# Performance work log

Measured on AMD Instinct MI355X. Metric: run time of the kernel, lower is better.

## Reference

```python
import jax, jax.numpy as jnp
import numpy as np

S, E, K, D = 50000, 20000, 128, 64
NUM_LAYER = 3
E1, E0 = 1000000, 1000000  # nnz of pos / neg adjacency
B = 4096


def _edges(key, n_rows, n_cols, n_edges):
    k1, k2, k3 = jax.random.split(key, 3)
    rows = jax.random.randint(k1, (n_edges,), 0, n_rows)
    cols = jax.random.randint(k2, (n_edges,), 0, n_cols)
    vals = jax.random.uniform(k3, (n_edges,), jnp.float32, 0.0, 0.1)
    return rows, cols, vals


def setup_inputs() -> dict:
    key = jax.random.key(0)
    ks = jax.random.split(key, 32)
    inp = {}
    inp['stu_id'] = jax.random.randint(ks[0], (B,), 0, S)
    inp['exer_id'] = jax.random.randint(ks[1], (B,), 0, E)
    inp['kn_emb'] = (jax.random.uniform(ks[2], (B, K)) < 0.1).astype(jnp.float32)
    # embeddings
    inp['stu_emb'] = jax.random.normal(ks[3], (S, D), jnp.float32) * 0.1
    inp['exer_emb'] = jax.random.normal(ks[4], (E, D), jnp.float32) * 0.1
    inp['kn_base'] = jax.random.normal(ks[5], (K, D), jnp.float32) * 0.1
    inp['stu_bias'] = jax.random.normal(ks[6], (S, 1), jnp.float32) * 0.1
    inp['e_disc'] = jax.random.normal(ks[7], (E, 1), jnp.float32) * 0.1
    # GCN linear layers
    inp['W1_w'] = jax.random.normal(ks[8], (K, K), jnp.float32) * (1.0 / np.sqrt(K))
    inp['W1_b'] = jnp.zeros((K,), jnp.float32)
    inp['W0_w'] = jax.random.normal(ks[9], (K, K), jnp.float32) * (1.0 / np.sqrt(K))
    inp['W0_b'] = jnp.zeros((K,), jnp.float32)
    # PosLinear prednet
    inp['pn1_w'] = jax.random.normal(ks[10], (256, K), jnp.float32) * 0.05
    inp['pn1_b'] = jnp.zeros((256,), jnp.float32)
    inp['pn2_w'] = jax.random.normal(ks[11], (128, 256), jnp.float32) * 0.05
    inp['pn2_b'] = jnp.zeros((128,), jnp.float32)
    inp['pn3_w'] = jax.random.normal(ks[12], (1, 128), jnp.float32) * 0.05
    inp['pn3_b'] = jnp.zeros((1,), jnp.float32)
    # sparse adjacencies (COO) pos(1) / neg(0), user->item and item->user
    r, c, v = _edges(ks[13], S, E, E1)
    inp['ui1_r'], inp['ui1_c'], inp['ui1_v'] = r, c, v
    r, c, v = _edges(ks[14], E, S, E1)
    inp['iu1_r'], inp['iu1_c'], inp['iu1_v'] = r, c, v
    r, c, v = _edges(ks[15], S, E, E0)
    inp['ui0_r'], inp['ui0_c'], inp['ui0_v'] = r, c, v
    r, c, v = _edges(ks[16], E, S, E0)
    inp['iu0_r'], inp['iu0_c'], inp['iu0_v'] = r, c, v
    # self-loop degree normalizers (1/(deg+1)-style positive scalars)
    inp['d_i_1'] = jax.random.uniform(ks[17], (S,), jnp.float32, 0.01, 1.0)
    inp['d_j_1'] = jax.random.uniform(ks[18], (E,), jnp.float32, 0.01, 1.0)
    inp['d_i_0'] = jax.random.uniform(ks[19], (S,), jnp.float32, 0.01, 1.0)
    inp['d_j_0'] = jax.random.uniform(ks[20], (E,), jnp.float32, 0.01, 1.0)
    return inp


def _spmm(rows, cols, vals, x, n_rows):
    # sparse [n_rows, n_cols] @ dense [n_cols, K]
    return jax.ops.segment_sum(vals[:, None] * x[cols], rows, num_segments=n_rows)


def _poslinear(x, w, b):
    wp = 2.0 * jax.nn.relu(-w) + w  # == |w|, as in PosLinear
    return x @ wp.T + b


def reference(stu_id, exer_id, kn_emb, stu_emb, exer_emb, kn_base, stu_bias, e_disc,
              W1_w, W1_b, W0_w, W0_b, pn1_w, pn1_b, pn2_w, pn2_b, pn3_w, pn3_b,
              ui1_r, ui1_c, ui1_v, iu1_r, iu1_c, iu1_v,
              ui0_r, ui0_c, ui0_v, iu0_r, iu0_c, iu0_v,
              d_i_1, d_j_1, d_i_0, d_j_0):
    # project embeddings onto knowledge space: [S,K], [E,K]
    stat = stu_emb @ kn_base.T
    kdiff = exer_emb @ kn_base.T
    for _ in range(NUM_LAYER):
        u1 = _spmm(ui1_r, ui1_c, ui1_v, kdiff, S) + stat * d_i_1[:, None]
        u1 = u1 @ W1_w.T + W1_b
        i1 = _spmm(iu1_r, iu1_c, iu1_v, stat, E) + kdiff * d_j_1[:, None]
        i1 = i1 @ W1_w.T + W1_b
        u0 = _spmm(ui0_r, ui0_c, ui0_v, kdiff, S) + stat * d_i_0[:, None]
        u0 = u0 @ W0_w.T + W0_b
        i0 = _spmm(iu0_r, iu0_c, iu0_v, stat, E) + kdiff * d_j_0[:, None]
        i0 = i0 @ W0_w.T + W0_b
        stat = u1 + u0
        kdiff = i1 + i0
    # diagnosis head (NCD-style), dropout in eval mode -> identity
    stat_b = jax.nn.sigmoid(stat[stu_id] + stu_bias[stu_id])      # [B,K]
    k_d = jax.nn.sigmoid(kdiff[exer_id])                           # [B,K]
    disc = jax.nn.sigmoid(e_disc[exer_id])                         # [B,1]
    x = disc * (stat_b - k_d) * kn_emb
    x = jax.nn.sigmoid(_poslinear(x, pn1_w, pn1_b))
    x = jax.nn.sigmoid(_poslinear(x, pn2_w, pn2_b))
    out = jax.nn.sigmoid(_poslinear(x, pn3_w, pn3_b)).reshape(-1)
    return out
```

## Files before the change

kernel.cpp:

```cpp
#include <hip/hip_runtime.h>
#include <hip/hip_bf16.h>

#define SN 50000
#define EN 20000
#define KN 128
#define DN 64
#define BN 4096
#define NE 1000000
#define NLAYER 3

#define CH_SHIFT 12
#define NCH0 5
#define NCH1 13
#define SIDE1_BASE2 (2 * SN * NCH0)
#define NTOT2 (2 * (SN * NCH0 + EN * NCH1))

#define BIN_SHIFT 11
#define NBIN2 ((NTOT2 + 2047) >> 11)
#define T1 4096
#define PG1 ((NE + T1 - 1) / T1)
#define HB 256

typedef float f32x4 __attribute__((ext_vector_type(4)));
typedef float f32x2 __attribute__((ext_vector_type(2)));
typedef short bf16x8 __attribute__((ext_vector_type(8)));

__device__ __forceinline__ float sigmoidf_(float v) { return 1.f / (1.f + __expf(-v)); }
__device__ __forceinline__ float bf_lo(unsigned u) { return __uint_as_float(u << 16); }
__device__ __forceinline__ float bf_hi(unsigned u) { return __uint_as_float(u & 0xffff0000u); }
__device__ __forceinline__ float bf_one(unsigned short s) { return __uint_as_float((unsigned)s << 16); }
__device__ __forceinline__ unsigned packbf2(float a, float b) {
    __hip_bfloat16 ha = __float2bfloat16(a), hb = __float2bfloat16(b);
    unsigned short ua = *(unsigned short*)&ha, ub = *(unsigned short*)&hb;
    return (unsigned)ua | ((unsigned)ub << 16);
}
__device__ __forceinline__ unsigned short packbf1(float a) {
    __hip_bfloat16 ha = __float2bfloat16(a);
    return *(unsigned short*)&ha;
}
__device__ __forceinline__ unsigned char fp8_of_bf16(unsigned short h) {
    float f = bf_one(h);
    int pk = __builtin_amdgcn_cvt_pk_fp8_f32(f, f, 0, false);
    return (unsigned char)(pk & 0xff);
}

struct CsrB {
    const int* rows[4]; const int* cols[4]; const float* vals[4];
};

__device__ __forceinline__ int bucket_idx(int a, int r, int cc) {
    int side = a >> 1;
    int nch = side ? NCH1 : NCH0;
    int base = side ? SIDE1_BASE2 : 0;
    int tb = a & 1;
    return base + (2 * r + tb) * nch + (cc >> CH_SHIFT);
}

__global__ __launch_bounds__(256) void hist_coarse(CsrB c, int* __restrict__ cnt) {
    __shared__ int h[512];
    const int t = threadIdx.x;
    h[t] = 0; h[t + 256] = 0;
    __syncthreads();
    const int a = blockIdx.x >> 8;
    const int tile = blockIdx.x & 255;
    const int per = (NE + HB - 1) / HB;
    const int beg = tile * per, end = min(beg + per, NE);
    for (int i = beg + t; i < end; i += 256)
        atomicAdd(&h[bucket_idx(a, c.rows[a][i], c.cols[a][i]) >> BIN_SHIFT], 1);
    __syncthreads();
    if (h[t]) atomicAdd(&cnt[t], h[t]);
    if (h[t + 256]) atomicAdd(&cnt[t + 256], h[t + 256]);
}

__global__ __launch_bounds__(512) void scan_coarse(const int* __restrict__ cnt,
                                                   int* __restrict__ base,
                                                   int* __restrict__ tails) {
    __shared__ int sh[512];
    const int t = threadIdx.x;
    const int v = (t < NBIN2) ? cnt[t] : 0;
    sh[t] = v;
    __syncthreads();
    for (int o = 1; o < 512; o <<= 1) {
        int x = sh[t]; int u = (t >= o) ? sh[t - o] : 0;
        __syncthreads(); sh[t] = x + u; __syncthreads();
    }
    if (t < NBIN2) {
        const int ex = sh[t] - v;
        base[t] = ex;
        tails[t] = ex;
    }
    if (t == 511) base[NBIN2] = sh[511];
}

__global__ __launch_bounds__(512) void part1(CsrB c, int* __restrict__ tails,
                                             int2* __restrict__ stg) {
    __shared__ int2 srec[T1];
    __shared__ unsigned short sbin[T1];
    __shared__ int h[512], offs[512], gbase[512], sc[512];
    const int t = threadIdx.x;
    const int a = blockIdx.x / PG1;
    const int tile = blockIdx.x - a * PG1;
    const int beg = tile * T1;
    const int cnt = min(T1, NE - beg);
    h[t] = 0;
    __syncthreads();

    int2 rec[8]; int rbin[8]; int rrank[8];
#pragma unroll
    for (int k = 0; k < 8; ++k) {
        int o = t + k * 512;
        if (o < cnt) {
            int i = beg + o;
            int cc = c.cols[a][i];
            int B = bucket_idx(a, c.rows[a][i], cc);
            int bin = B >> BIN_SHIFT;
            rec[k] = make_int2(cc | ((B & 2047) << 17), __float_as_int(c.vals[a][i]));
            rbin[k] = bin;
            rrank[k] = atomicAdd(&h[bin], 1);
        } else {
            rbin[k] = -1;
        }
    }
    __syncthreads();
    sc[t] = h[t];
    __syncthreads();
    for (int o = 1; o < 512; o <<= 1) {
        int x = sc[t]; int u = (t >= o) ? sc[t - o] : 0;
        __syncthreads(); sc[t] = x + u; __syncthreads();
    }
    offs[t] = sc[t] - h[t];
    if (h[t] > 0) gbase[t] = atomicAdd(&tails[t], h[t]);
    __syncthreads();
#pragma unroll
    for (int k = 0; k < 8; ++k) {
        if (rbin[k] >= 0) {
            int pos = offs[rbin[k]] + rrank[k];
            srec[pos] = rec[k];
            sbin[pos] = (unsigned short)rbin[k];
        }
    }
    __syncthreads();
    for (int idx = t; idx < cnt; idx += 512) {
        int b = sbin[idx];
        stg[gbase[b] + (idx - offs[b])] = srec[idx];
    }
}

__global__ __launch_bounds__(512) void part2(const int* __restrict__ coarseBase,
                                             const int2* __restrict__ stg,
                                             int* __restrict__ rp,
                                             int2* __restrict__ cv) {
    __shared__ int cnt2[2048];
    __shared__ int tsum[512];
    const int b = blockIdx.x;
    const int t = threadIdx.x;
    const int fineBase = b << BIN_SHIFT;
    const int nf = min(2048, NTOT2 - fineBase);
    const int segBeg = coarseBase[b];
    const int segEnd = coarseBase[b + 1];
    for (int i = t; i < 2048; i += 512) cnt2[i] = 0;
    __syncthreads();
    for (int e = segBeg + t; e < segEnd; e += 512)
        atomicAdd(&cnt2[((unsigned)stg[e].x) >> 17], 1);
    __syncthreads();
    const int i4 = t * 4;
    int v0 = cnt2[i4], v1 = cnt2[i4 + 1], v2 = cnt2[i4 + 2], v3 = cnt2[i4 + 3];
    tsum[t] = v0 + v1 + v2 + v3;
    __syncthreads();
    for (int o = 1; o < 512; o <<= 1) {
        int x = tsum[t]; int u = (t >= o) ? tsum[t - o] : 0;
        __syncthreads(); tsum[t] = x + u; __syncthreads();
    }
    const int pre = (t == 0) ? 0 : tsum[t - 1];
    const int p0 = pre, p1 = pre + v0, p2 = p1 + v1, p3 = p2 + v2;
    cnt2[i4] = p0; cnt2[i4 + 1] = p1; cnt2[i4 + 2] = p2; cnt2[i4 + 3] = p3;
    if (i4 + 0 < nf) rp[fineBase + i4 + 0] = segBeg + p0;
    if (i4 + 1 < nf) rp[fineBase + i4 + 1] = segBeg + p1;
    if (i4 + 2 < nf) rp[fineBase + i4 + 2] = segBeg + p2;
    if (i4 + 3 < nf) rp[fineBase + i4 + 3] = segBeg + p3;
    if (b == NBIN2 - 1 && t == 511) rp[NTOT2] = segEnd;
    __syncthreads();
    for (int e = segBeg + t; e < segEnd; e += 512) {
        int2 r = stg[e];
        int pos = segBeg + atomicAdd(&cnt2[((unsigned)r.x) >> 17], 1);
        cv[pos] = make_int2(r.x & 0xFFFF, r.y);
    }
}

__global__ __launch_bounds__(256) void f2bf3(
    const float* __restrict__ s0, unsigned short* __restrict__ d0, int n0,
    const float* __restrict__ s1, unsigned short* __restrict__ d1, int n1,
    const float* __restrict__ s2, unsigned short* __restrict__ d2, int n2) {
    int j = blockIdx.x * 256 + threadIdx.x;
    const float* s; unsigned short* d;
    if (j < n0) { s = s0; d = d0; }
    else {
        j -= n0;
        if (j < n1) { s = s1; d = d1; }
        else {
            j -= n1;
            if (j >= n2) return;
            s = s2; d = d2;
        }
    }
    float2 f = ((const float2*)s)[j];
    ((unsigned*)d)[j] = packbf2(f.x, f.y);
}

template <int KK>
__global__ __launch_bounds__(256) void gemm_proj(const float* __restrict__ X,
                                                 const unsigned short* __restrict__ W,
                                                 unsigned short* __restrict__ out,
                                                 unsigned char* __restrict__ f8,
                                                 int M) {
    constexpr int PITCH = KK + 8;
    __shared__ unsigned short Wl[128 * PITCH];
    const int t = threadIdx.x;
    for (int idx = t * 8; idx < 128 * KK; idx += 2048) {
        int r = idx / KK, k = idx - r * KK;
        *(uint4*)(&Wl[r * PITCH + k]) = *(const uint4*)(&W[idx]);
    }
    __syncthreads();
    const int lane = t & 63;
    const int nm = lane & 15;
    const int quad = lane >> 4;
    const int row0 = blockIdx.x * 64 + (t >> 6) * 16;
    if (row0 >= M) return;

    f32x4 acc[8];
#pragma unroll
    for (int nt = 0; nt < 8; ++nt) acc[nt] = (f32x4){0.f, 0.f, 0.f, 0.f};

    const float* xrow = X + (size_t)(row0 + nm) * KK + quad * 8;
#pragma unroll
    for (int ks = 0; ks < KK / 32; ++ks) {
        float4 f0 = *(const float4*)(xrow + ks * 32);
        float4 f1 = *(const float4*)(xrow + ks * 32 + 4);
        unsigned q[4] = {packbf2(f0.x, f0.y), packbf2(f0.z, f0.w),
                         packbf2(f1.x, f1.y), packbf2(f1.z, f1.w)};
        bf16x8 a = *(bf16x8*)q;
#pragma unroll
        for (int nt = 0; nt < 8; ++nt) {
            bf16x8 b = *(const bf16x8*)(&Wl[(nt * 16 + nm) * PITCH + ks * 32 + quad * 8]);
            acc[nt] = __builtin_amdgcn_mfma_f32_16x16x32_bf16(a, b, acc[nt], 0, 0, 0);
        }
    }
    const size_t obase = (size_t)(row0 + quad * 4) * 128 + nm;
    unsigned short* orow = out + obase;
    unsigned char* frow = f8 + obase;
#pragma unroll
    for (int r = 0; r < 4; ++r)
#pragma unroll
        for (int nt = 0; nt < 8; ++nt) {
            unsigned short h = packbf1(acc[nt][r]);
            orow[(size_t)r * 128 + nt * 16] = h;
            frow[(size_t)r * 128 + nt * 16] = fp8_of_bf16(h);
        }
}

template <bool LIST>
__global__ __launch_bounds__(512) void gemm2_mfma(
    const unsigned short* __restrict__ agg1S, const unsigned short* __restrict__ agg0S,
    const unsigned short* __restrict__ yS,
    const float* __restrict__ d1S, const float* __restrict__ d0S,
    unsigned short* __restrict__ outS, unsigned char* __restrict__ f8S,
    const unsigned short* __restrict__ agg1E, const unsigned short* __restrict__ agg0E,
    const unsigned short* __restrict__ yE,
    const float* __restrict__ d1E, const float* __restrict__ d0E,
    unsigned short* __restrict__ outE, unsigned char* __restrict__ f8E,
    const unsigned short* __restrict__ W1, const unsigned short* __restrict__ W0,
    const float* __restrict__ b1, const float* __restrict__ b0,
    const int* __restrict__ idsS, const int* __restrict__ idsE, int nblkS) {
    constexpr int PITCH = 136;
    __shared__ unsigned short Wl[2 * 128 * PITCH];
    const int t = threadIdx.x;
    for (int idx = t * 8; idx < 128 * 128; idx += 4096) {
        int r = idx >> 7, k = idx & 127;
        *(uint4*)(&Wl[r * PITCH + k]) = *(const uint4*)(&W1[idx]);
        *(uint4*)(&Wl[128 * PITCH + r * PITCH + k]) = *(const uint4*)(&W0[idx]);
    }
    __syncthreads();
    const bool sideE = (int)blockIdx.x >= nblkS;
    const unsigned short* agg1 = sideE ? agg1E : agg1S;
    const unsigned short* agg0 = sideE ? agg0E : agg0S;
    const unsigned short* y    = sideE ? yE : yS;
    const float* d1 = sideE ? d1E : d1S;
    const float* d0 = sideE ? d0E : d0S;
    unsigned short* out = sideE ? outE : outS;
    unsigned char* f8 = sideE ? f8E : f8S;
    const int M = LIST ? BN : (sideE ? EN : SN);
    const int lane = t & 63;
    const int nm = lane & 15;
    const int quad = lane >> 4;
    const int row0 = ((int)blockIdx.x - (sideE ? nblkS : 0)) * 128 + (t >> 6) * 16;
    if (row0 >= M) return;

    const int lrow = row0 + nm;
    int grow = lrow;
    if (LIST) grow = (sideE ? idsE : idsS)[lrow];

    const float d1v = d1[grow];
    const float d0v = d0[grow];

    f32x4 acc[8];
#pragma unroll
    for (int nt = 0; nt < 8; ++nt) acc[nt] = (f32x4){0.f, 0.f, 0.f, 0.f};

    const size_t rbA = (size_t)lrow * 128 + quad * 8;
    const size_t rbY = (size_t)grow * 128 + quad * 8;
#pragma unroll
    for (int ks = 0; ks < 4; ++ks) {
        uint4 ua1 = *(const uint4*)(agg1 + rbA + ks * 32);
        uint4 ua0 = *(const uint4*)(agg0 + rbA + ks * 32);
        uint4 uy  = *(const uint4*)(y    + rbY + ks * 32);
        uint4 p1, p0;
        {
            unsigned* a1 = (unsigned*)&ua1; unsigned* a0 = (unsigned*)&ua0;
            unsigned* yy = (unsigned*)&uy;
            unsigned* q1 = (unsigned*)&p1; unsigned* q0 = (unsigned*)&p0;
#pragma unroll
            for (int w = 0; w < 4; ++w) {
                float ylo = bf_lo(yy[w]), yhi = bf_hi(yy[w]);
                q1[w] = packbf2(bf_lo(a1[w]) + d1v * ylo, bf_hi(a1[w]) + d1v * yhi);
                q0[w] = packbf2(bf_lo(a0[w]) + d0v * ylo, bf_hi(a0[w]) + d0v * yhi);
            }
        }
        bf16x8 af1 = *(bf16x8*)&p1;
        bf16x8 af0 = *(bf16x8*)&p0;
#pragma unroll
        for (int nt = 0; nt < 8; ++nt) {
            bf16x8 bw1 = *(const bf16x8*)(&Wl[(nt * 16 + nm) * PITCH + ks * 32 + quad * 8]);
            acc[nt] = __builtin_amdgcn_mfma_f32_16x16x32_bf16(af1, bw1, acc[nt], 0, 0, 0);
            bf16x8 bw0 = *(const bf16x8*)(&Wl[128 * PITCH + (nt * 16 + nm) * PITCH + ks * 32 + quad * 8]);
            acc[nt] = __builtin_amdgcn_mfma_f32_16x16x32_bf16(af0, bw0, acc[nt], 0, 0, 0);
        }
    }
    const size_t obase = (size_t)(row0 + quad * 4) * 128 + nm;
    unsigned short* orow = out + obase;
    unsigned char* frow = f8 + obase;
#pragma unroll
    for (int nt = 0; nt < 8; ++nt) {
        float bb = b1[nt * 16 + nm] + b0[nt * 16 + nm];
#pragma unroll
        for (int r = 0; r < 4; ++r) {
            unsigned short h = packbf1(acc[nt][r] + bb);
            orow[(size_t)r * 128 + nt * 16] = h;
            if (!LIST) frow[(size_t)r * 128 + nt * 16] = fp8_of_bf16(h);
        }
    }
}

template <bool LIST>
__global__ __launch_bounds__(256) void spmm_all(
    const int* __restrict__ rp, const long long* __restrict__ cv,
    const unsigned char* __restrict__ kd8, const unsigned char* __restrict__ st8,
    unsigned short* __restrict__ as1, unsigned short* __restrict__ as0,
    unsigned short* __restrict__ ae1, unsigned short* __restrict__ ae0,
    const int* __restrict__ idsS, const int* __restrict__ idsE) {
    const int wave = (blockIdx.x * 256 + threadIdx.x) >> 6;
    const int lane = threadIdx.x & 63;
    const int NW = LIST ? 2 * BN : SN + EN;
    if (wave >= NW) return;
    const bool sideE = LIST ? (wave >= BN) : (wave >= SN);
    const int li = sideE ? (wave - (LIST ? BN : SN)) : wave;
    const int r = LIST ? (sideE ? idsE[li] : idsS[li]) : li;
    const int nch = sideE ? NCH1 : NCH0;
    const int* rpb = rp + (sideE ? SIDE1_BASE2 : 0);
    const int q = lane >> 4;
    const int c = lane & 15;
    const unsigned char* g8 = (sideE ? st8 : kd8) + c * 8;

    const int rbase = 2 * r * nch;
    const int e0 = rpb[rbase];
    const int em = rpb[rbase + nch];
    const int ee = rpb[rbase + 2 * nch];

    f32x2 accP[4], accN[4];
#pragma unroll
    for (int j = 0; j < 4; ++j) { accP[j] = (f32x2){0.f, 0.f}; accN[j] = (f32x2){0.f, 0.f}; }

#define QUAD(E, ACC)                                                        \
    {                                                                       \
        int col = (int)((E) & 0xFFFF);                                      \
        float v = __int_as_float((int)((E) >> 32));                         \
        f32x2 vv = {v, v};                                                  \
        uint2 u = *(const uint2*)(g8 + (col << 7));                         \
        ACC[0] += vv * __builtin_amdgcn_cvt_pk_f32_fp8((int)u.x, false);    \
        ACC[1] += vv * __builtin_amdgcn_cvt_pk_f32_fp8((int)u.x, true);     \
        ACC[2] += vv * __builtin_amdgcn_cvt_pk_f32_fp8((int)u.y, false);    \
        ACC[3] += vv * __builtin_amdgcn_cvt_pk_f32_fp8((int)u.y, true);     \
    }

    {
        int e = e0;
        for (; e + 16 <= em; e += 16) {
            long long E0 = cv[e + q];
            long long E1 = cv[e + 4 + q];
            long long E2 = cv[e + 8 + q];
            long long E3 = cv[e + 12 + q];
            QUAD(E0, accP) QUAD(E1, accP) QUAD(E2, accP) QUAD(E3, accP)
        }
        for (; e + 4 <= em; e += 4) {
            long long E0 = cv[e + q];
            QUAD(E0, accP)
        }
        if (e < em) {
            int idx = min(e + q, em - 1);
            long long E0 = cv[idx];
            if (e + q >= em) E0 &= 0xFFFFLL;
            QUAD(E0, accP)
        }
    }
    {
        int e = em;
        for (; e + 16 <= ee; e += 16) {
            long long E0 = cv[e + q];
            long long E1 = cv[e + 4 + q];
            long long E2 = cv[e + 8 + q];
            long long E3 = cv[e + 12 + q];
            QUAD(E0, accN) QUAD(E1, accN) QUAD(E2, accN) QUAD(E3, accN)
        }
        for (; e + 4 <= ee; e += 4) {
            long long E0 = cv[e + q];
            QUAD(E0, accN)
        }
        if (e < ee) {
            int idx = min(e + q, ee - 1);
            long long E0 = cv[idx];
            if (e + q >= ee) E0 &= 0xFFFFLL;
            QUAD(E0, accN)
        }
    }
#undef QUAD

#pragma unroll
    for (int j = 0; j < 4; ++j) {
        accP[j].x += __shfl_xor(accP[j].x, 16);
        accP[j].y += __shfl_xor(accP[j].y, 16);
        accN[j].x += __shfl_xor(accN[j].x, 16);
        accN[j].y += __shfl_xor(accN[j].y, 16);
        accP[j].x += __shfl_xor(accP[j].x, 32);
        accP[j].y += __shfl_xor(accP[j].y, 32);
        accN[j].x += __shfl_xor(accN[j].x, 32);
        accN[j].y += __shfl_xor(accN[j].y, 32);
    }
    unsigned short* o1 = sideE ? ae1 : as1;
    unsigned short* o0 = sideE ? ae0 : as0;
    const int oi = LIST ? li : r;
    const int base = (oi << 7) + c * 8;
    if (q == 0) {
        uint4 w;
        w.x = packbf2(accP[0].x, accP[0].y);
        w.y = packbf2(accP[1].x, accP[1].y);
        w.z = packbf2(accP[2].x, accP[2].y);
        w.w = packbf2(accP[3].x, accP[3].y);
        *(uint4*)&o1[base] = w;
    } else if (q == 1) {
        uint4 w;
        w.x = packbf2(accN[0].x, accN[0].y);
        w.y = packbf2(accN[1].x, accN[1].y);
        w.z = packbf2(accN[2].x, accN[2].y);
        w.w = packbf2(accN[3].x, accN[3].y);
        *(uint4*)&o0[base] = w;
    }
}

template <int KK, int NCOLS, int ROWS, bool ABSW, bool SIG>
__global__ __launch_bounds__(256) void gemm_xwT(const float* __restrict__ X,
                                                const float* __restrict__ W,
                                                const float* __restrict__ bias,
                                                float* __restrict__ out, int M) {
    constexpr int KP = 32;
    constexpr int NG = 256 / NCOLS;
    constexpr int RT = ROWS / NG;
    __shared__ float BT[KP * (NCOLS + 1)];
    __shared__ float Xl[ROWS * (KK + 1)];
    const int t = threadIdx.x;
    const int j = t % NCOLS;
    const int rg = t / NCOLS;
    const int row0 = blockIdx.x * ROWS;

    for (int idx = t; idx < ROWS * KK; idx += 256) {
        int r = idx / KK, k = idx % KK;
        int gr = row0 + r;
        Xl[r * (KK + 1) + k] = (gr < M) ? X[gr * KK + k] : 0.f;
    }
    float acc[RT];
#pragma unroll
    for (int i = 0; i < RT; ++i) acc[i] = 0.f;

    for (int k0 = 0; k0 < KK; k0 += KP) {
        __syncthreads();
        for (int idx = t; idx < NCOLS * KP; idx += 256) {
            int jj = idx / KP, kp = idx % KP;
            float w = W[jj * KK + k0 + kp];
            BT[kp * (NCOLS + 1) + jj] = ABSW ? fabsf(w) : w;
        }
        __syncthreads();
#pragma unroll
        for (int kp = 0; kp < KP; ++kp) {
            float b = BT[kp * (NCOLS + 1) + j];
#pragma unroll
            for (int rr = 0; rr < RT; ++rr)
                acc[rr] += Xl[(rg * RT + rr) * (KK + 1) + k0 + kp] * b;
        }
    }
    float bj = bias ? bias[j] : 0.f;
#pragma unroll
    for (int rr = 0; rr < RT; ++rr) {
        int gr = row0 + rg * RT + rr;
        if (gr < M) {
            float v = acc[rr] + bj;
            out[gr * NCOLS + j] = SIG ? sigmoidf_(v) : v;
        }
    }
}

__global__ __launch_bounds__(128) void head1_kernel(
    const int* __restrict__ stu_id, const int* __restrict__ exer_id,
    const float* __restrict__ kn_emb, const unsigned short* __restrict__ statB,
    const unsigned short* __restrict__ kdB, const float* __restrict__ stu_bias,
    const float* __restrict__ e_disc, float* __restrict__ x) {
    const int b = blockIdx.x;
    const int k = threadIdx.x;
    const int sid = stu_id[b], eid = exer_id[b];
    float disc = sigmoidf_(e_disc[eid]);
    float sb = sigmoidf_(bf_one(statB[(b << 7) + k]) + stu_bias[sid]);
    float kd = sigmoidf_(bf_one(kdB[(b << 7) + k]));
    x[(b << 7) + k] = disc * (sb - kd) * kn_emb[(b << 7) + k];
}

__global__ __launch_bounds__(256) void pn3_kernel(const float* __restrict__ h2,
                                                  const float* __restrict__ w3,
                                                  const float* __restrict__ b3,
                                                  float* __restrict__ out) {
    __shared__ float wl[128];
    const int t = threadIdx.x;
    if (t < 128) wl[t] = fabsf(w3[t]);
    __syncthreads();
    const int b = blockIdx.x * 256 + t;
    float acc = 0.f;
#pragma unroll 4
    for (int k = 0; k < 128; ++k) acc += h2[(b << 7) + k] * wl[k];
    out[b] = sigmoidf_(acc + b3[0]);
}

static inline size_t align256(size_t x) { return (x + 255) & ~size_t(255); }

extern "C" void kernel_launch(void* const* d_in, const int* in_sizes, int n_in,
                              void* d_out, int out_size, void* d_ws, size_t ws_size,
                              hipStream_t stream) {
    const int*   stu_id   = (const int*)d_in[0];
    const int*   exer_id  = (const int*)d_in[1];
    const float* kn_emb   = (const float*)d_in[2];
    const float* stu_emb  = (const float*)d_in[3];
    const float* exer_emb = (const float*)d_in[4];
    const float* kn_base  = (const float*)d_in[5];
    const float* stu_bias = (const float*)d_in[6];
    const float* e_disc   = (const float*)d_in[7];
    const float* W1_w     = (const float*)d_in[8];
    const float* W1_b     = (const float*)d_in[9];
    const float* W0_w     = (const float*)d_in[10];
    const float* W0_b     = (const float*)d_in[11];
    const float* pn1_w    = (const float*)d_in[12];
    const float* pn1_b    = (const float*)d_in[13];
    const float* pn2_w    = (const float*)d_in[14];
    const float* pn2_b    = (const float*)d_in[15];
    const float* pn3_w    = (const float*)d_in[16];
    const float* pn3_b    = (const float*)d_in[17];
    const int*   ui1_r = (const int*)d_in[18]; const int* ui1_c = (const int*)d_in[19];
    const float* ui1_v = (const float*)d_in[20];
    const int*   iu1_r = (const int*)d_in[21]; const int* iu1_c = (const int*)d_in[22];
    const float* iu1_v = (const float*)d_in[23];
    const int*   ui0_r = (const int*)d_in[24]; const int* ui0_c = (const int*)d_in[25];
    const float* ui0_v = (const float*)d_in[26];
    const int*   iu0_r = (const int*)d_in[27]; const int* iu0_c = (const int*)d_in[28];
    const float* iu0_v = (const float*)d_in[29];
    const float* d_i_1 = (const float*)d_in[30];
    const float* d_j_1 = (const float*)d_in[31];
    const float* d_i_0 = (const float*)d_in[32];
    const float* d_j_0 = (const float*)d_in[33];
    float* out = (float*)d_out;

    typedef unsigned short u16;
    typedef unsigned char u8;
    char* p = (char*)d_ws;
    size_t off = 0;
    auto alloc = [&](size_t bytes) { char* q = p + off; off += align256(bytes); return q; };
    u16* stat  = (u16*)alloc(size_t(SN) * KN * 2);
    u16* kdiff = (u16*)alloc(size_t(EN) * KN * 2);
    u8* st8 = (u8*)alloc(size_t(SN) * KN);
    u8* kd8 = (u8*)alloc(size_t(EN) * KN);
    u16* as1 = (u16*)alloc(size_t(SN) * KN * 2);
    u16* as0 = (u16*)alloc(size_t(SN) * KN * 2);
    u16* ae1 = (u16*)alloc(size_t(EN) * KN * 2);
    u16* ae0 = (u16*)alloc(size_t(EN) * KN * 2);
    u16* statB = (u16*)alloc(size_t(BN) * KN * 2);
    u16* kdB   = (u16*)alloc(size_t(BN) * KN * 2);
    u16* Kb  = (u16*)alloc(size_t(KN) * DN * 2);
    u16* Wb1 = (u16*)alloc(size_t(KN) * KN * 2);
    u16* Wb0 = (u16*)alloc(size_t(KN) * KN * 2);
    int*  coarseCnt  = (int*)alloc(512 * 4);
    int*  coarseBase = (int*)alloc((NBIN2 + 1) * 4);
    int*  tails      = (int*)alloc(512 * 4);
    int*  rp_all     = (int*)alloc(size_t(NTOT2 + 1) * 4);
    int2* stg        = (int2*)alloc(size_t(4) * NE * 8);
    int2* cv_all     = (int2*)alloc(size_t(4) * NE * 8);
    float* xh = (float*)alloc(size_t(BN) * KN * 4);
    float* h1 = (float*)alloc(size_t(BN) * 256 * 4);
    float* h2 = (float*)alloc(size_t(BN) * 128 * 4);
    if (off > ws_size) return;

    CsrB c;
    c.rows[0] = ui1_r; c.cols[0] = ui1_c; c.vals[0] = ui1_v;
    c.rows[1] = ui0_r; c.cols[1] = ui0_c; c.vals[1] = ui0_v;
    c.rows[2] = iu1_r; c.cols[2] = iu1_c; c.vals[2] = iu1_v;
    c.rows[3] = iu0_r; c.cols[3] = iu0_c; c.vals[3] = iu0_v;

    hipMemsetAsync(coarseCnt, 0, 512 * 4, stream);
    hist_coarse<<<4 * HB, 256, 0, stream>>>(c, coarseCnt);
    scan_coarse<<<1, 512, 0, stream>>>(coarseCnt, coarseBase, tails);
    part1<<<4 * PG1, 512, 0, stream>>>(c, tails, stg);
    part2<<<NBIN2, 512, 0, stream>>>(coarseBase, stg, rp_all, cv_all);

    {
        const int n0 = KN * DN / 2, n1 = KN * KN / 2, n2 = KN * KN / 2;
        f2bf3<<<(n0 + n1 + n2 + 255) / 256, 256, 0, stream>>>(
            kn_base, Kb, n0, W1_w, Wb1, n1, W0_w, Wb0, n2);
    }

    gemm_proj<DN><<<(SN + 63) / 64, 256, 0, stream>>>(stu_emb, Kb, stat, st8, SN);
    gemm_proj<DN><<<(EN + 63) / 64, 256, 0, stream>>>(exer_emb, Kb, kdiff, kd8, EN);

    const int nblkS = (SN + 127) / 128, nblkE = (EN + 127) / 128;

    for (int l = 0; l < NLAYER; ++l) {
        if (l < NLAYER - 1) {
            spmm_all<false><<<(SN + EN + 3) / 4, 256, 0, stream>>>(
                rp_all, (const long long*)cv_all, kd8, st8, as1, as0, ae1, ae0,
                nullptr, nullptr);
            gemm2_mfma<false><<<nblkS + nblkE, 512, 0, stream>>>(
                as1, as0, stat, d_i_1, d_i_0, stat, st8,
                ae1, ae0, kdiff, d_j_1, d_j_0, kdiff, kd8,
                Wb1, Wb0, W1_b, W0_b, nullptr, nullptr, nblkS);
        } else {
            spmm_all<true><<<(2 * BN) / 4, 256, 0, stream>>>(
                rp_all, (const long long*)cv_all, kd8, st8, as1, as0, ae1, ae0,
                stu_id, exer_id);
            gemm2_mfma<true><<<2 * (BN / 128), 512, 0, stream>>>(
                as1, as0, stat, d_i_1, d_i_0, statB, nullptr,
                ae1, ae0, kdiff, d_j_1, d_j_0, kdB, nullptr,
                Wb1, Wb0, W1_b, W0_b, stu_id, exer_id, BN / 128);
        }
    }

    head1_kernel<<<BN, 128, 0, stream>>>(stu_id, exer_id, kn_emb, statB, kdB,
                                         stu_bias, e_disc, xh);
    gemm_xwT<128, 256, 16, true, true><<<BN / 16, 256, 0, stream>>>(xh, pn1_w, pn1_b, h1, BN);
    gemm_xwT<256, 128, 32, true, true><<<BN / 32, 256, 0, stream>>>(h1, pn2_w, pn2_b, h2, BN);
    pn3_kernel<<<BN / 256, 256, 0, stream>>>(h2, pn3_w, pn3_b, out);
    (void)out_size; (void)n_in; (void)in_sizes;
}
```

Measured before the change: 607.1 us.

## Fuse head kernels, merge projection GEMMs, fold memset into weight conversion

Folds the coarse-count memset into the weight-to-bf16 conversion kernel and merges the two projection GEMM launches into one grid covering both the student and exercise sides. Fuses the head elementwise step into the first prednet GEMM and the third linear layer into the second GEMM, which drops the xh and h2 intermediate buffers. The aim is fewer kernel launches and less global traffic in the small tail stages, at the cost of some extra shared memory and per-block work in the fused kernels.

```diff
diff --git a/kernel.cpp b/kernel.cpp
--- a/kernel.cpp
+++ b/kernel.cpp
@@ -187,11 +187,13 @@
     }
 }
 
-__global__ __launch_bounds__(256) void f2bf3(
+__global__ __launch_bounds__(256) void f2bf3z(
     const float* __restrict__ s0, unsigned short* __restrict__ d0, int n0,
     const float* __restrict__ s1, unsigned short* __restrict__ d1, int n1,
-    const float* __restrict__ s2, unsigned short* __restrict__ d2, int n2) {
+    const float* __restrict__ s2, unsigned short* __restrict__ d2, int n2,
+    int* __restrict__ coarseCnt) {
     int j = blockIdx.x * 256 + threadIdx.x;
+    if (j < 512) coarseCnt[j] = 0;
     const float* s; unsigned short* d;
     if (j < n0) { s = s0; d = d0; }
     else {
@@ -208,11 +210,12 @@
 }
 
 template <int KK>
-__global__ __launch_bounds__(256) void gemm_proj(const float* __restrict__ X,
-                                                 const unsigned short* __restrict__ W,
-                                                 unsigned short* __restrict__ out,
-                                                 unsigned char* __restrict__ f8,
-                                                 int M) {
+__global__ __launch_bounds__(256) void gemm_proj2(
+    const float* __restrict__ XS, const float* __restrict__ XE,
+    const unsigned short* __restrict__ W,
+    unsigned short* __restrict__ outS, unsigned char* __restrict__ f8S,
+    unsigned short* __restrict__ outE, unsigned char* __restrict__ f8E,
+    int nbS) {
     constexpr int PITCH = KK + 8;
     __shared__ unsigned short Wl[128 * PITCH];
     const int t = threadIdx.x;
@@ -221,10 +224,15 @@
         *(uint4*)(&Wl[r * PITCH + k]) = *(const uint4*)(&W[idx]);
     }
     __syncthreads();
+    const bool sideE = (int)blockIdx.x >= nbS;
+    const float* X = sideE ? XE : XS;
+    unsigned short* out = sideE ? outE : outS;
+    unsigned char* f8 = sideE ? f8E : f8S;
+    const int M = sideE ? EN : SN;
     const int lane = t & 63;
     const int nm = lane & 15;
     const int quad = lane >> 4;
-    const int row0 = blockIdx.x * 64 + (t >> 6) * 16;
+    const int row0 = ((int)blockIdx.x - (sideE ? nbS : 0)) * 64 + (t >> 6) * 16;
     if (row0 >= M) return;
 
     f32x4 acc[8];
@@ -465,26 +473,34 @@
     }
 }
 
-template <int KK, int NCOLS, int ROWS, bool ABSW, bool SIG>
-__global__ __launch_bounds__(256) void gemm_xwT(const float* __restrict__ X,
-                                                const float* __restrict__ W,
-                                                const float* __restrict__ bias,
-                                                float* __restrict__ out, int M) {
-    constexpr int KP = 32;
-    constexpr int NG = 256 / NCOLS;
-    constexpr int RT = ROWS / NG;
+__global__ __launch_bounds__(256) void pn1_fused(
+    const int* __restrict__ stu_id, const int* __restrict__ exer_id,
+    const float* __restrict__ kn_emb, const unsigned short* __restrict__ statB,
+    const unsigned short* __restrict__ kdB, const float* __restrict__ stu_bias,
+    const float* __restrict__ e_disc,
+    const float* __restrict__ W, const float* __restrict__ bias,
+    float* __restrict__ out) {
+    constexpr int KK = 128, NCOLS = 256, ROWS = 16, KP = 32;
+    constexpr int RT = 16;
     __shared__ float BT[KP * (NCOLS + 1)];
     __shared__ float Xl[ROWS * (KK + 1)];
-    const int t = threadIdx.x;
-    const int j = t % NCOLS;
-    const int rg = t / NCOLS;
+    __shared__ float sdisc[16], sbias[16];
+    const int t = threadIdx.x;
     const int row0 = blockIdx.x * ROWS;
-
+    if (t < 16) {
+        const int gr = row0 + t;
+        sdisc[t] = sigmoidf_(e_disc[exer_id[gr]]);
+        sbias[t] = stu_bias[stu_id[gr]];
+    }
+    __syncthreads();
     for (int idx = t; idx < ROWS * KK; idx += 256) {
-        int r = idx / KK, k = idx % KK;
-        int gr = row0 + r;
-        Xl[r * (KK + 1) + k] = (gr < M) ? X[gr * KK + k] : 0.f;
-    }
+        const int r = idx >> 7, k = idx & 127;
+        const int gr = row0 + r;
+        const float sb = sigmoidf_(bf_one(statB[(gr << 7) + k]) + sbias[r]);
+        const float kd = sigmoidf_(bf_one(kdB[(gr << 7) + k]));
+        Xl[r * (KK + 1) + k] = sdisc[r] * (sb - kd) * kn_emb[(gr << 7) + k];
+    }
+    const int j = t;
     float acc[RT];
 #pragma unroll
     for (int i = 0; i < RT; ++i) acc[i] = 0.f;
@@ -493,8 +509,7 @@
         __syncthreads();
         for (int idx = t; idx < NCOLS * KP; idx += 256) {
             int jj = idx / KP, kp = idx % KP;
-            float w = W[jj * KK + k0 + kp];
-            BT[kp * (NCOLS + 1) + jj] = ABSW ? fabsf(w) : w;
+            BT[kp * (NCOLS + 1) + jj] = fabsf(W[jj * KK + k0 + kp]);
         }
         __syncthreads();
 #pragma unroll
@@ -502,47 +517,65 @@
             float b = BT[kp * (NCOLS + 1) + j];
 #pragma unroll
             for (int rr = 0; rr < RT; ++rr)
+                acc[rr] += Xl[rr * (KK + 1) + k0 + kp] * b;
+        }
+    }
+    const float bj = bias[j];
+#pragma unroll
+    for (int rr = 0; rr < RT; ++rr)
+        out[(row0 + rr) * NCOLS + j] = sigmoidf_(acc[rr] + bj);
+}
+
+__global__ __launch_bounds__(256) void pn23_fused(
+    const float* __restrict__ X, const float* __restrict__ W,
+    const float* __restrict__ bias, const float* __restrict__ w3,
+    const float* __restrict__ b3, float* __restrict__ out) {
+    constexpr int KK = 256, NCOLS = 128, ROWS = 32, KP = 32;
+    constexpr int RT = 16;
+    __shared__ float BT[KP * (NCOLS + 1)];
+    __shared__ float Xl[ROWS * (KK + 1)];
+    __shared__ float Sv[ROWS][NCOLS + 1];
+    __shared__ float wl[128];
+    const int t = threadIdx.x;
+    const int j = t % NCOLS;
+    const int rg = t / NCOLS;
+    const int row0 = blockIdx.x * ROWS;
+    if (t < 128) wl[t] = fabsf(w3[t]);
+
+    for (int idx = t; idx < ROWS * KK; idx += 256) {
+        const int r = idx >> 8, k = idx & 255;
+        Xl[r * (KK + 1) + k] = X[(row0 + r) * KK + k];
+    }
+    float acc[RT];
+#pragma unroll
+    for (int i = 0; i < RT; ++i) acc[i] = 0.f;
+
+    for (int k0 = 0; k0 < KK; k0 += KP) {
+        __syncthreads();
+        for (int idx = t; idx < NCOLS * KP; idx += 256) {
+            int jj = idx / KP, kp = idx % KP;
+            BT[kp * (NCOLS + 1) + jj] = fabsf(W[jj * KK + k0 + kp]);
+        }
+        __syncthreads();
+#pragma unroll
+        for (int kp = 0; kp < KP; ++kp) {
+            float b = BT[kp * (NCOLS + 1) + j];
+#pragma unroll
+            for (int rr = 0; rr < RT; ++rr)
                 acc[rr] += Xl[(rg * RT + rr) * (KK + 1) + k0 + kp] * b;
         }
     }
-    float bj = bias ? bias[j] : 0.f;
-#pragma unroll
-    for (int rr = 0; rr < RT; ++rr) {
-        int gr = row0 + rg * RT + rr;
-        if (gr < M) {
-            float v = acc[rr] + bj;
-            out[gr * NCOLS + j] = SIG ? sigmoidf_(v) : v;
-        }
-    }
-}
-
-__global__ __launch_bounds__(128) void head1_kernel(
-    const int* __restrict__ stu_id, const int* __restrict__ exer_id,
-    const float* __restrict__ kn_emb, const unsigned short* __restrict__ statB,
-    const unsigned short* __restrict__ kdB, const float* __restrict__ stu_bias,
-    const float* __restrict__ e_disc, float* __restrict__ x) {
-    const int b = blockIdx.x;
-    const int k = threadIdx.x;
-    const int sid = stu_id[b], eid = exer_id[b];
-    float disc = sigmoidf_(e_disc[eid]);
-    float sb = sigmoidf_(bf_one(statB[(b << 7) + k]) + stu_bias[sid]);
-    float kd = sigmoidf_(bf_one(kdB[(b << 7) + k]));
-    x[(b << 7) + k] = disc * (sb - kd) * kn_emb[(b << 7) + k];
-}
-
-__global__ __launch_bounds__(256) void pn3_kernel(const float* __restrict__ h2,
-                                                  const float* __restrict__ w3,
-                                                  const float* __restrict__ b3,
-                                                  float* __restrict__ out) {
-    __shared__ float wl[128];
-    const int t = threadIdx.x;
-    if (t < 128) wl[t] = fabsf(w3[t]);
-    __syncthreads();
-    const int b = blockIdx.x * 256 + t;
-    float acc = 0.f;
+    const float bj = bias[j];
+#pragma unroll
+    for (int rr = 0; rr < RT; ++rr)
+        Sv[rg * RT + rr][j] = sigmoidf_(acc[rr] + bj);
+    __syncthreads();
+    if (t < ROWS) {
+        float a = 0.f;
 #pragma unroll 4
-    for (int k = 0; k < 128; ++k) acc += h2[(b << 7) + k] * wl[k];
-    out[b] = sigmoidf_(acc + b3[0]);
+        for (int k = 0; k < 128; ++k) a += Sv[t][k] * wl[k];
+        out[row0 + t] = sigmoidf_(a + b3[0]);
+    }
 }
 
 static inline size_t align256(size_t x) { return (x + 255) & ~size_t(255); }
@@ -606,9 +639,7 @@
     int*  rp_all     = (int*)alloc(size_t(NTOT2 + 1) * 4);
     int2* stg        = (int2*)alloc(size_t(4) * NE * 8);
     int2* cv_all     = (int2*)alloc(size_t(4) * NE * 8);
-    float* xh = (float*)alloc(size_t(BN) * KN * 4);
     float* h1 = (float*)alloc(size_t(BN) * 256 * 4);
-    float* h2 = (float*)alloc(size_t(BN) * 128 * 4);
     if (off > ws_size) return;
 
     CsrB c;
@@ -617,20 +648,20 @@
     c.rows[2] = iu1_r; c.cols[2] = iu1_c; c.vals[2] = iu1_v;
     c.rows[3] = iu0_r; c.cols[3] = iu0_c; c.vals[3] = iu0_v;
 
-    hipMemsetAsync(coarseCnt, 0, 512 * 4, stream);
+    {
+        const int n0 = KN * DN / 2, n1 = KN * KN / 2, n2 = KN * KN / 2;
+        f2bf3z<<<(n0 + n1 + n2 + 255) / 256, 256, 0, stream>>>(
+            kn_base, Kb, n0, W1_w, Wb1, n1, W0_w, Wb0, n2, coarseCnt);
+    }
+
     hist_coarse<<<4 * HB, 256, 0, stream>>>(c, coarseCnt);
     scan_coarse<<<1, 512, 0, stream>>>(coarseCnt, coarseBase, tails);
     part1<<<4 * PG1, 512, 0, stream>>>(c, tails, stg);
     part2<<<NBIN2, 512, 0, stream>>>(coarseBase, stg, rp_all, cv_all);
 
-    {
-        const int n0 = KN * DN / 2, n1 = KN * KN / 2, n2 = KN * KN / 2;
-        f2bf3<<<(n0 + n1 + n2 + 255) / 256, 256, 0, stream>>>(
-            kn_base, Kb, n0, W1_w, Wb1, n1, W0_w, Wb0, n2);
-    }
-
-    gemm_proj<DN><<<(SN + 63) / 64, 256, 0, stream>>>(stu_emb, Kb, stat, st8, SN);
-    gemm_proj<DN><<<(EN + 63) / 64, 256, 0, stream>>>(exer_emb, Kb, kdiff, kd8, EN);
+    const int nbS = (SN + 63) / 64, nbE = (EN + 63) / 64;
+    gemm_proj2<DN><<<nbS + nbE, 256, 0, stream>>>(stu_emb, exer_emb, Kb,
+                                                  stat, st8, kdiff, kd8, nbS);
 
     const int nblkS = (SN + 127) / 128, nblkE = (EN + 127) / 128;
 
@@ -654,10 +685,8 @@
         }
     }
 
-    head1_kernel<<<BN, 128, 0, stream>>>(stu_id, exer_id, kn_emb, statB, kdB,
-                                         stu_bias, e_disc, xh);
-    gemm_xwT<128, 256, 16, true, true><<<BN / 16, 256, 0, stream>>>(xh, pn1_w, pn1_b, h1, BN);
-    gemm_xwT<256, 128, 32, true, true><<<BN / 32, 256, 0, stream>>>(h1, pn2_w, pn2_b, h2, BN);
-    pn3_kernel<<<BN / 256, 256, 0, stream>>>(h2, pn3_w, pn3_b, out);
+    pn1_fused<<<BN / 16, 256, 0, stream>>>(stu_id, exer_id, kn_emb, statB, kdB,
+                                           stu_bias, e_disc, pn1_w, pn1_b, h1);
+    pn23_fused<<<BN / 32, 256, 0, stream>>>(h1, pn2_w, pn2_b, pn3_w, pn3_b, out);
     (void)out_size; (void)n_in; (void)in_sizes;
 }
```

Result: faster. 571.4 us (-5.9%).
